# Performance work log

Hardware: AMD Instinct MI355X
Metric: run time of the kernel (lower is better)

Reference implementation:

```python
import jax, jax.numpy as jnp
import numpy as np


def setup_inputs() -> dict:
    key = jax.random.key(0)
    k1, k2, k3, k4 = jax.random.split(key, 4)
    B, Cin, Cout, K, Wd, H, Wsp = 16, 256, 256, 3, 256, 64, 64
    fan_in = Cin * K * K
    return {
        "x": jax.random.normal(k1, (B, Cin, H, Wsp), dtype=jnp.float32),
        "w": jax.random.normal(k2, (B, Wd), dtype=jnp.float32),
        "conv_weight": jax.random.normal(k3, (Cout, Cin, K, K), dtype=jnp.float32) * 0.05,
        "style_w": jax.random.normal(k4, (Cin, Wd), dtype=jnp.float32) * 0.05,
        "style_b": jnp.zeros((Cin,), dtype=jnp.float32),
        "scale": jnp.asarray(1.0 / np.sqrt(fan_in), dtype=jnp.float32),
    }


def reference(x, w, conv_weight, style_w, style_b, scale):
    # x: [B, Cin, H, W]; w: [B, Wd]; conv_weight: [Cout, Cin, K, K]
    B, Cin, H, Wsp = x.shape
    Cout, _, K, _ = conv_weight.shape
    # style modulation: s = Linear(w) -> [B, 1, Cin, 1, 1]
    s = (w @ style_w.T + style_b).reshape(B, 1, Cin, 1, 1)
    # modulate + demodulate per-sample weights: [B, Cout, Cin, K, K]
    wt = (conv_weight * scale)[None] * s
    demod = jax.lax.rsqrt(jnp.sum(wt * wt, axis=(2, 3, 4), keepdims=True) + 1e-8)
    wt = (wt * demod).reshape(B * Cout, Cin, K, K)
    # grouped conv emulation: input [1, B*Cin, H, W], groups=B
    xr = x.reshape(1, B * Cin, H, Wsp)
    pad = 1
    out = jax.lax.conv_general_dilated(
        xr, wt,
        window_strides=(1, 1),
        padding=[(pad, pad), (pad, pad)],
        dimension_numbers=("NCHW", "OIHW", "NCHW"),
        feature_group_count=B,
    )
    return out.reshape(B, Cout, out.shape[2], out.shape[3])
```

## Files before the change

### kernel.cpp

```cpp
#include <hip/hip_runtime.h>
#include <hip/hip_bf16.h>

#define BB   16
#define CIN  256
#define COUT 256
#define WD   256
#define HH   64
#define WWS  64
#define NSP  4096
#define KW   9

typedef __attribute__((ext_vector_type(8))) short short8;
typedef __attribute__((ext_vector_type(4))) float f32x4;
typedef unsigned short ushort_t;

#define S_BYTES (BB*CIN*4)
#define WT_OFF (S_BYTES)
#define WT_BYTES (BB*9*COUT*CIN*2)
#define X_OFF (WT_OFF + WT_BYTES)
#define X_BYTES (BB*NSP*CIN*2)
#define ZP_OFF (X_OFF + X_BYTES)
#define ZP_BYTES 4096
#define WS_NEEDED ((size_t)(ZP_OFF + ZP_BYTES))

#define WAITVM2 asm volatile("s_waitcnt vmcnt(2)" ::: "memory")
#define WAITVM8 asm volatile("s_waitcnt vmcnt(8)" ::: "memory")

__device__ inline ushort_t f2bf(float f) {
    __hip_bfloat16 h = __float2bfloat16(f);
    return __builtin_bit_cast(ushort_t, h);
}

__device__ inline void gload_lds16(const ushort_t* g, ushort_t* l) {
    __builtin_amdgcn_global_load_lds(
        (const __attribute__((address_space(1))) void*)g,
        (__attribute__((address_space(3))) void*)l, 16, 0, 0);
}

__global__ __launch_bounds__(256)
void zero_kernel(float* __restrict__ zp) {
    ((float4*)zp)[threadIdx.x] = make_float4(0.f, 0.f, 0.f, 0.f);
}

__global__ __launch_bounds__(256)
void style_kernel(const float* __restrict__ w,
                  const float* __restrict__ style_w,
                  const float* __restrict__ style_b,
                  float* __restrict__ s) {
    const int b  = blockIdx.x;
    const int ci = threadIdx.x;
    __shared__ float wsh[WD];
    wsh[ci] = w[b * WD + ci];
    __syncthreads();
    const float* row = style_w + ci * WD;
    float acc = style_b[ci];
    #pragma unroll 4
    for (int k = 0; k < WD; ++k) acc += wsh[k] * row[k];
    s[b * CIN + ci] = acc;
}

__global__ __launch_bounds__(256)
void wt_kernel(const float* __restrict__ cw, const float* __restrict__ s,
               const float* __restrict__ scale_p, ushort_t* __restrict__ wt) {
    const int co = blockIdx.x, b = blockIdx.y, ci = threadIdx.x;
    const float sv = s[b * CIN + ci] * scale_p[0];
    const float* cp = cw + ((size_t)co * CIN + ci) * KW;
    float v[9];
    float ss = 0.f;
    #pragma unroll
    for (int t = 0; t < 9; ++t) { v[t] = cp[t] * sv; ss += v[t] * v[t]; }
    #pragma unroll
    for (int off = 32; off > 0; off >>= 1) ss += __shfl_down(ss, off);
    __shared__ float red[4];
    if ((ci & 63) == 0) red[ci >> 6] = ss;
    __syncthreads();
    const float dm = rsqrtf(red[0] + red[1] + red[2] + red[3] + 1e-8f);
    #pragma unroll
    for (int t = 0; t < 9; ++t)
        wt[((size_t)(b * 9 + t) * COUT + co) * CIN + ci] = f2bf(v[t] * dm);
}

__global__ __launch_bounds__(256)
void xpose_kernel(const float* __restrict__ x, ushort_t* __restrict__ xo) {
    const int spt = blockIdx.x;
    const int cit = blockIdx.y;
    const int b   = blockIdx.z;
    const int t   = threadIdx.x;
    __shared__ ushort_t tile[64 * 68];
    const int sp0 = spt * 64, ci0 = cit * 64;
    {
        const int spq = t & 15, cil = t >> 4;
        #pragma unroll
        for (int i = 0; i < 4; ++i) {
            const int ci = cil + i * 16;
            const float4 v = *(const float4*)(x + ((size_t)(b * CIN + ci0 + ci)) * NSP + sp0 + spq * 4);
            tile[(spq * 4 + 0) * 68 + ci] = f2bf(v.x);
            tile[(spq * 4 + 1) * 68 + ci] = f2bf(v.y);
            tile[(spq * 4 + 2) * 68 + ci] = f2bf(v.z);
            tile[(spq * 4 + 3) * 68 + ci] = f2bf(v.w);
        }
    }
    __syncthreads();
    {
        const int g4 = t & 15, sp = t >> 4;
        #pragma unroll
        for (int i = 0; i < 4; ++i) {
            const int spp = sp + i * 16;
            uint2 v = *(const uint2*)&tile[spp * 68 + g4 * 4];
            *(uint2*)(xo + ((size_t)(b * NSP + sp0 + spp)) * CIN + ci0 + g4 * 4) = v;
        }
    }
}

__global__ __launch_bounds__(256, 2)
void conv_mfma_kernel(const ushort_t* __restrict__ wt,
                      const ushort_t* __restrict__ xo,
                      const ushort_t* __restrict__ zp,
                      float* __restrict__ out) {
    const int wg = blockIdx.x;
    const int b  = (wg & 7) + 8 * ((wg >> 3) & 1);
    const int cohalf = (wg >> 4) & 1;
    const int ntile  = wg >> 5;
    const int y0 = ntile * 4;

    const int tid  = threadIdx.x;
    const int lane = tid & 63;
    const int w    = tid >> 6;
    const int wm   = w >> 1;
    const int wn   = w & 1;
    const int l15  = lane & 15;
    const int lg   = lane >> 4;
    const int q    = lane >> 2;

    __shared__ __align__(16) ushort_t lds_a[3 * 128 * 32];
    __shared__ __align__(16) ushort_t lds_x[2 * 6 * 66 * 32];

    const int srcq8 = (((lane & 3) ^ ((q ^ (q >> 2)) & 3))) * 8;

    const long wtb = (long)b * 9 * COUT * CIN;
    const ushort_t* pa0 = wt + wtb + (long)(cohalf * 128 + w * 16 + q) * CIN + srcq8;
    const ushort_t* pa1 = pa0 + 64 * CIN;
    const int aluni0 = w * 512;
    const int aluni1 = 2048 + w * 512;

    const ushort_t* px[6];
    int xdst_off[6];
    #pragma unroll
    for (int j = 0; j < 6; ++j) {
        const int s  = w * 6 + j;
        const int r  = s >> 2;
        const int cq = s & 3;
        const int y  = y0 - 1 + r;
        const bool val = (y >= 0 && y < HH);
        const int cp = cq * 16 + q;
        px[j] = val ? (xo + ((long)b * NSP + (long)y * WWS + cp) * CIN + srcq8)
                    : (zp + lane * 8);
        xdst_off[j] = r * 2112 + cq * 512 + 32;
    }

    const int slotA8 = (lg ^ ((l15 ^ (l15 >> 2)) & 3)) * 8;
    int slotB8[3];
    #pragma unroll
    for (int kx = 0; kx < 3; ++kx) {
        int c2 = l15 + kx - 1;
        if (c2 < 0) c2 = 0;
        slotB8[kx] = (lg ^ ((c2 ^ (c2 >> 2)) & 3)) * 8;
    }
    const int abase = (wm * 64 + l15) * 32 + slotA8;

    f32x4 acc[4][8];
    #pragma unroll
    for (int mi = 0; mi < 4; ++mi)
        #pragma unroll
        for (int ni = 0; ni < 8; ++ni) acc[mi][ni] = (f32x4){0.f, 0.f, 0.f, 0.f};

    if (tid < 96) {
        const int cell = tid >> 2, qq = tid & 3;
        const int buf = cell / 12, cr = cell % 12;
        const int r = cr >> 1, col = (cr & 1) * 65;
        *(uint4*)&lds_x[buf * 12672 + r * 2112 + col * 32 + qq * 8] =
            make_uint4(0, 0, 0, 0);
    }

    #pragma unroll
    for (int j = 0; j < 6; ++j)
        gload_lds16(px[j], lds_x + xdst_off[j]);
    gload_lds16(pa0, lds_a + aluni0);
    gload_lds16(pa1, lds_a + aluni1);
    gload_lds16(pa0 + (long)COUT * CIN, lds_a + 4096 + aluni0);
    gload_lds16(pa1 + (long)COUT * CIN, lds_a + 4096 + aluni1);

    asm volatile("s_waitcnt lgkmcnt(0)" ::: "memory");

    for (int chunk = 0; chunk < 8; ++chunk) {
        const ushort_t* xb = lds_x + (chunk & 1) * 12672;

        #pragma unroll
        for (int tap = 0; tap < 9; ++tap) {
            if (tap == 1 || tap == 2) { WAITVM8; } else { WAITVM2; }
            __builtin_amdgcn_sched_barrier(0);
            __builtin_amdgcn_s_barrier();

            {
                const int tp2 = (tap + 2) % 9;
                const int ch2 = (tap >= 7) ? ((chunk + 1) & 7) : chunk;
                const long aoff = (long)tp2 * (COUT * CIN) + ch2 * 32;
                ushort_t* adst = lds_a + ((tap + 2) % 3) * 4096;
                gload_lds16(pa0 + aoff, adst + aluni0);
                gload_lds16(pa1 + aoff, adst + aluni1);
            }
            if (tap == 0) {
                const int cs = (chunk + 1) & 7;
                ushort_t* xdst = lds_x + ((chunk + 1) & 1) * 12672;
                #pragma unroll
                for (int j = 0; j < 6; ++j)
                    gload_lds16(px[j] + cs * 32, xdst + xdst_off[j]);
            }

            const int ky = tap / 3, kx = tap % 3;
            const ushort_t* ab = lds_a + (tap % 3) * 4096 + abase;
            short8 af[4];
            #pragma unroll
            for (int mi = 0; mi < 4; ++mi) af[mi] = *(const short8*)(ab + mi * 512);
            short8 bf[8];
            #pragma unroll
            for (int ni = 0; ni < 8; ++ni) {
                const int row = wn * 2 + (ni >> 2) + ky;
                const int col = (ni & 3) * 16 + l15 + kx;
                bf[ni] = *(const short8*)(xb + row * 2112 + col * 32 + slotB8[kx]);
            }

            __builtin_amdgcn_s_setprio(1);
            #pragma unroll
            for (int mi = 0; mi < 4; ++mi)
                #pragma unroll
                for (int ni = 0; ni < 8; ++ni)
                    acc[mi][ni] = __builtin_amdgcn_mfma_f32_16x16x32_bf16(
                        af[mi], bf[ni], acc[mi][ni], 0, 0, 0);
            __builtin_amdgcn_s_setprio(0);
        }
    }

    const int co_b = cohalf * 128 + wm * 64 + lg * 4;
    const int sp_b = ntile * 256 + wn * 128 + l15;
    #pragma unroll
    for (int mi = 0; mi < 4; ++mi)
        #pragma unroll
        for (int ni = 0; ni < 8; ++ni)
            #pragma unroll
            for (int rg = 0; rg < 4; ++rg) {
                const int co = co_b + mi * 16 + rg;
                const int sp = sp_b + ni * 16;
                out[((long)(b * COUT + co)) * NSP + sp] = acc[mi][ni][rg];
            }
}

__global__ __launch_bounds__(256)
void modconv_kernel(const float* __restrict__ x,
                    const float* __restrict__ cw,
                    const float* __restrict__ s,
                    const float* __restrict__ scale_p,
                    float* __restrict__ out) {
    const int tile = blockIdx.x;
    const int co   = blockIdx.y;
    const int b    = blockIdx.z;
    const int tid  = threadIdx.x;
    const float scale = scale_p[0];

    __shared__ float s_wt[CIN * KW];
    __shared__ float s_x[18 * 66];
    __shared__ float red[4];

    const float* cwb = cw + (size_t)co * CIN * KW;
    const float* sb  = s + b * CIN;
    float sumsq = 0.f;
    for (int i = tid; i < CIN * KW; i += 256) {
        float v = cwb[i] * scale * sb[i / KW];
        s_wt[i] = v;
        sumsq += v * v;
    }
    #pragma unroll
    for (int off = 32; off > 0; off >>= 1) sumsq += __shfl_down(sumsq, off);
    if ((tid & 63) == 0) red[tid >> 6] = sumsq;
    __syncthreads();
    const float demod = rsqrtf(red[0] + red[1] + red[2] + red[3] + 1e-8f);
    for (int i = tid; i < CIN * KW; i += 256) s_wt[i] *= demod;

    const int tx = tid & 63;
    const int tr = tid >> 6;
    const int y0 = tile * 16;
    float acc[4] = {0.f, 0.f, 0.f, 0.f};

    for (int ci = 0; ci < CIN; ++ci) {
        __syncthreads();
        const float* xb = x + ((size_t)(b * CIN + ci)) * (HH * WWS);
        for (int idx = tid; idx < 18 * 66; idx += 256) {
            const int r = idx / 66, c = idx % 66;
            const int yg = y0 - 1 + r, xg = c - 1;
            float v = 0.f;
            if (yg >= 0 && yg < HH && xg >= 0 && xg < WWS) v = xb[yg * WWS + xg];
            s_x[idx] = v;
        }
        __syncthreads();
        const float* wr = s_wt + ci * KW;
        const float w0 = wr[0], w1 = wr[1], w2 = wr[2];
        const float w3 = wr[3], w4 = wr[4], w5 = wr[5];
        const float w6 = wr[6], w7 = wr[7], w8 = wr[8];
        const int rbase = tr * 4;
        float xv[6][3];
        #pragma unroll
        for (int j = 0; j < 6; ++j)
            #pragma unroll
            for (int k = 0; k < 3; ++k) xv[j][k] = s_x[(rbase + j) * 66 + tx + k];
        #pragma unroll
        for (int i = 0; i < 4; ++i)
            acc[i] += w0 * xv[i][0] + w1 * xv[i][1] + w2 * xv[i][2]
                    + w3 * xv[i+1][0] + w4 * xv[i+1][1] + w5 * xv[i+1][2]
                    + w6 * xv[i+2][0] + w7 * xv[i+2][1] + w8 * xv[i+2][2];
    }
    float* ob = out + (((size_t)(b * COUT + co)) * HH + y0) * WWS + tx;
    #pragma unroll
    for (int i = 0; i < 4; ++i) ob[(tr * 4 + i) * WWS] = acc[i];
}

extern "C" void kernel_launch(void* const* d_in, const int* in_sizes, int n_in,
                              void* d_out, int out_size, void* d_ws, size_t ws_size,
                              hipStream_t stream) {
    const float* x       = (const float*)d_in[0];
    const float* w       = (const float*)d_in[1];
    const float* cw      = (const float*)d_in[2];
    const float* style_w = (const float*)d_in[3];
    const float* style_b = (const float*)d_in[4];
    const float* scale_p = (const float*)d_in[5];
    float*       out     = (float*)d_out;

    float*    s    = (float*)d_ws;
    ushort_t* wswt = (ushort_t*)((char*)d_ws + WT_OFF);
    ushort_t* wsx  = (ushort_t*)((char*)d_ws + X_OFF);
    float*    zp   = (float*)((char*)d_ws + ZP_OFF);

    style_kernel<<<dim3(BB), 256, 0, stream>>>(w, style_w, style_b, s);

    if (ws_size >= WS_NEEDED) {
        zero_kernel<<<dim3(1), 256, 0, stream>>>(zp);
        wt_kernel<<<dim3(COUT, BB), 256, 0, stream>>>(cw, s, scale_p, wswt);
        xpose_kernel<<<dim3(64, 4, BB), 256, 0, stream>>>(x, wsx);
        conv_mfma_kernel<<<dim3(512), 256, 0, stream>>>(wswt, wsx,
                                                        (const ushort_t*)zp, out);
    } else {
        modconv_kernel<<<dim3(4, COUT, BB), 256, 0, stream>>>(x, cw, s, scale_p, out);
    }
}
```

Measured before the change: 108.7 us.

## Enlarge conv tile to all 256 output channels per workgroup with vectorized stores

Each workgroup now computes all 256 output channels for its spatial tile instead of half, so the input halo tile is loaded once per spatial tile rather than twice, and the grid halves to 256 workgroups. Each wave holds a 128x128 accumulator block, which raises register pressure and drops occupancy to one workgroup per SIMD set. The MFMA operands are swapped so each lane holds four consecutive spatial outputs, which turns the epilogue into 16-byte vector stores. Wait counts and LDS buffer sizes are adjusted for the doubled weight loads.

Result: slower. 131.4 us (+20.8%).

```diff
diff --git a/kernel.cpp b/kernel.cpp
--- a/kernel.cpp
+++ b/kernel.cpp
@@ -23,8 +23,8 @@
 #define ZP_BYTES 4096
 #define WS_NEEDED ((size_t)(ZP_OFF + ZP_BYTES))
 
-#define WAITVM2 asm volatile("s_waitcnt vmcnt(2)" ::: "memory")
-#define WAITVM8 asm volatile("s_waitcnt vmcnt(8)" ::: "memory")
+#define WAITVM4  asm volatile("s_waitcnt vmcnt(4)" ::: "memory")
+#define WAITVM10 asm volatile("s_waitcnt vmcnt(10)" ::: "memory")
 
 __device__ inline ushort_t f2bf(float f) {
     __hip_bfloat16 h = __float2bfloat16(f);
@@ -112,15 +112,14 @@
     }
 }
 
-__global__ __launch_bounds__(256, 2)
+__global__ __launch_bounds__(256, 1)
 void conv_mfma_kernel(const ushort_t* __restrict__ wt,
                       const ushort_t* __restrict__ xo,
                       const ushort_t* __restrict__ zp,
                       float* __restrict__ out) {
     const int wg = blockIdx.x;
-    const int b  = (wg & 7) + 8 * ((wg >> 3) & 1);
-    const int cohalf = (wg >> 4) & 1;
-    const int ntile  = wg >> 5;
+    const int b  = (wg & 7) | ((wg >> 7) << 3);
+    const int ntile = (wg >> 3) & 15;
     const int y0 = ntile * 4;
 
     const int tid  = threadIdx.x;
@@ -132,16 +131,19 @@
     const int lg   = lane >> 4;
     const int q    = lane >> 2;
 
-    __shared__ __align__(16) ushort_t lds_a[3 * 128 * 32];
+    __shared__ __align__(16) ushort_t lds_a[3 * 256 * 32];
     __shared__ __align__(16) ushort_t lds_x[2 * 6 * 66 * 32];
 
     const int srcq8 = (((lane & 3) ^ ((q ^ (q >> 2)) & 3))) * 8;
 
     const long wtb = (long)b * 9 * COUT * CIN;
-    const ushort_t* pa0 = wt + wtb + (long)(cohalf * 128 + w * 16 + q) * CIN + srcq8;
-    const ushort_t* pa1 = pa0 + 64 * CIN;
-    const int aluni0 = w * 512;
-    const int aluni1 = 2048 + w * 512;
+    const ushort_t* pa[4];
+    int aluni[4];
+    #pragma unroll
+    for (int i = 0; i < 4; ++i) {
+        pa[i] = wt + wtb + (long)(i * 64 + w * 16 + q) * CIN + srcq8;
+        aluni[i] = i * 2048 + w * 512;
+    }
 
     const ushort_t* px[6];
     int xdst_off[6];
@@ -166,11 +168,11 @@
         if (c2 < 0) c2 = 0;
         slotB8[kx] = (lg ^ ((c2 ^ (c2 >> 2)) & 3)) * 8;
     }
-    const int abase = (wm * 64 + l15) * 32 + slotA8;
-
-    f32x4 acc[4][8];
-    #pragma unroll
-    for (int mi = 0; mi < 4; ++mi)
+    const int abase = (wm * 128 + l15) * 32 + slotA8;
+
+    f32x4 acc[8][8];
+    #pragma unroll
+    for (int mi = 0; mi < 8; ++mi)
         #pragma unroll
         for (int ni = 0; ni < 8; ++ni) acc[mi][ni] = (f32x4){0.f, 0.f, 0.f, 0.f};
 
@@ -181,23 +183,25 @@
         *(uint4*)&lds_x[buf * 12672 + r * 2112 + col * 32 + qq * 8] =
             make_uint4(0, 0, 0, 0);
     }
+    asm volatile("s_waitcnt lgkmcnt(0)" ::: "memory");
+    __builtin_amdgcn_sched_barrier(0);
 
     #pragma unroll
     for (int j = 0; j < 6; ++j)
         gload_lds16(px[j], lds_x + xdst_off[j]);
-    gload_lds16(pa0, lds_a + aluni0);
-    gload_lds16(pa1, lds_a + aluni1);
-    gload_lds16(pa0 + (long)COUT * CIN, lds_a + 4096 + aluni0);
-    gload_lds16(pa1 + (long)COUT * CIN, lds_a + 4096 + aluni1);
-
-    asm volatile("s_waitcnt lgkmcnt(0)" ::: "memory");
+    #pragma unroll
+    for (int i = 0; i < 4; ++i)
+        gload_lds16(pa[i], lds_a + aluni[i]);
+    #pragma unroll
+    for (int i = 0; i < 4; ++i)
+        gload_lds16(pa[i] + (long)COUT * CIN, lds_a + 8192 + aluni[i]);
 
     for (int chunk = 0; chunk < 8; ++chunk) {
         const ushort_t* xb = lds_x + (chunk & 1) * 12672;
 
         #pragma unroll
         for (int tap = 0; tap < 9; ++tap) {
-            if (tap == 1 || tap == 2) { WAITVM8; } else { WAITVM2; }
+            if (tap == 1 || tap == 2) { WAITVM10; } else { WAITVM4; }
             __builtin_amdgcn_sched_barrier(0);
             __builtin_amdgcn_s_barrier();
 
@@ -205,9 +209,10 @@
                 const int tp2 = (tap + 2) % 9;
                 const int ch2 = (tap >= 7) ? ((chunk + 1) & 7) : chunk;
                 const long aoff = (long)tp2 * (COUT * CIN) + ch2 * 32;
-                ushort_t* adst = lds_a + ((tap + 2) % 3) * 4096;
-                gload_lds16(pa0 + aoff, adst + aluni0);
-                gload_lds16(pa1 + aoff, adst + aluni1);
+                ushort_t* adst = lds_a + ((tap + 2) % 3) * 8192;
+                #pragma unroll
+                for (int i = 0; i < 4; ++i)
+                    gload_lds16(pa[i] + aoff, adst + aluni[i]);
             }
             if (tap == 0) {
                 const int cs = (chunk + 1) & 7;
@@ -218,10 +223,10 @@
             }
 
             const int ky = tap / 3, kx = tap % 3;
-            const ushort_t* ab = lds_a + (tap % 3) * 4096 + abase;
-            short8 af[4];
+            const ushort_t* ab = lds_a + (tap % 3) * 8192 + abase;
+            short8 af[8];
             #pragma unroll
-            for (int mi = 0; mi < 4; ++mi) af[mi] = *(const short8*)(ab + mi * 512);
+            for (int mi = 0; mi < 8; ++mi) af[mi] = *(const short8*)(ab + mi * 512);
             short8 bf[8];
             #pragma unroll
             for (int ni = 0; ni < 8; ++ni) {
@@ -232,27 +237,24 @@
 
             __builtin_amdgcn_s_setprio(1);
             #pragma unroll
-            for (int mi = 0; mi < 4; ++mi)
+            for (int mi = 0; mi < 8; ++mi)
                 #pragma unroll
                 for (int ni = 0; ni < 8; ++ni)
                     acc[mi][ni] = __builtin_amdgcn_mfma_f32_16x16x32_bf16(
-                        af[mi], bf[ni], acc[mi][ni], 0, 0, 0);
+                        bf[ni], af[mi], acc[mi][ni], 0, 0, 0);
             __builtin_amdgcn_s_setprio(0);
         }
     }
 
-    const int co_b = cohalf * 128 + wm * 64 + lg * 4;
-    const int sp_b = ntile * 256 + wn * 128 + l15;
-    #pragma unroll
-    for (int mi = 0; mi < 4; ++mi)
+    #pragma unroll
+    for (int mi = 0; mi < 8; ++mi) {
+        const int co = wm * 128 + mi * 16 + l15;
+        float* ob = out + ((long)(b * COUT + co)) * NSP
+                  + ntile * 256 + wn * 128 + lg * 4;
         #pragma unroll
         for (int ni = 0; ni < 8; ++ni)
-            #pragma unroll
-            for (int rg = 0; rg < 4; ++rg) {
-                const int co = co_b + mi * 16 + rg;
-                const int sp = sp_b + ni * 16;
-                out[((long)(b * COUT + co)) * NSP + sp] = acc[mi][ni][rg];
-            }
+            *(f32x4*)(ob + ni * 16) = acc[mi][ni];
+    }
 }
 
 __global__ __launch_bounds__(256)
@@ -345,7 +347,7 @@
         zero_kernel<<<dim3(1), 256, 0, stream>>>(zp);
         wt_kernel<<<dim3(COUT, BB), 256, 0, stream>>>(cw, s, scale_p, wswt);
         xpose_kernel<<<dim3(64, 4, BB), 256, 0, stream>>>(x, wsx);
-        conv_mfma_kernel<<<dim3(512), 256, 0, stream>>>(wswt, wsx,
+        conv_mfma_kernel<<<dim3(256), 256, 0, stream>>>(wswt, wsx,
                                                         (const ushort_t*)zp, out);
     } else {
         modconv_kernel<<<dim3(4, COUT, BB), 256, 0, stream>>>(x, cw, s, scale_p, out);
```

## Split conv workgroup across 8 waves with smaller per-wave tiles and vector stores

Applied to the files above, without the earlier changes.

Doubles the conv kernel's workgroup to 512 threads (8 waves), halving each wave's accumulator tile to 4x4 MFMA blocks and the number of async global-to-LDS loads per thread. The MFMA operands are swapped so each lane holds four consecutive spatial outputs, which lets the epilogue write 16-byte vector stores instead of scalar ones. The vmcnt wait counts are lowered to match the fewer in-flight loads. This aims for more latency hiding and less register pressure, at the cost of more barrier participants and less register-level reuse per wave.

After: 110.3 us. No clear change (+1.5%).

```diff
diff --git a/kernel.cpp b/kernel.cpp
--- a/kernel.cpp
+++ b/kernel.cpp
@@ -23,8 +23,8 @@
 #define ZP_BYTES 4096
 #define WS_NEEDED ((size_t)(ZP_OFF + ZP_BYTES))
 
-#define WAITVM2 asm volatile("s_waitcnt vmcnt(2)" ::: "memory")
-#define WAITVM8 asm volatile("s_waitcnt vmcnt(8)" ::: "memory")
+#define WAITVM1 asm volatile("s_waitcnt vmcnt(1)" ::: "memory")
+#define WAITVM4 asm volatile("s_waitcnt vmcnt(4)" ::: "memory")
 
 __device__ inline ushort_t f2bf(float f) {
     __hip_bfloat16 h = __float2bfloat16(f);
@@ -112,22 +112,23 @@
     }
 }
 
-__global__ __launch_bounds__(256, 2)
+__global__ __launch_bounds__(512, 4)
 void conv_mfma_kernel(const ushort_t* __restrict__ wt,
                       const ushort_t* __restrict__ xo,
                       const ushort_t* __restrict__ zp,
                       float* __restrict__ out) {
     const int wg = blockIdx.x;
-    const int b  = (wg & 7) + 8 * ((wg >> 3) & 1);
-    const int cohalf = (wg >> 4) & 1;
-    const int ntile  = wg >> 5;
+    const int b  = (wg & 7) | (((wg >> 3) & 1) << 3);
+    const int r2 = wg >> 4;
+    const int cohalf = r2 & 1;
+    const int ntile  = r2 >> 1;
     const int y0 = ntile * 4;
 
     const int tid  = threadIdx.x;
     const int lane = tid & 63;
     const int w    = tid >> 6;
-    const int wm   = w >> 1;
-    const int wn   = w & 1;
+    const int wm   = w >> 2;
+    const int wn   = w & 3;
     const int l15  = lane & 15;
     const int lg   = lane >> 4;
     const int q    = lane >> 2;
@@ -135,27 +136,25 @@
     __shared__ __align__(16) ushort_t lds_a[3 * 128 * 32];
     __shared__ __align__(16) ushort_t lds_x[2 * 6 * 66 * 32];
 
-    const int srcq8 = (((lane & 3) ^ ((q ^ (q >> 2)) & 3))) * 8;
-
+    const int srcqA8 = ((lane & 3) ^ ((q ^ (q >> 2)) & 3)) * 8;
     const long wtb = (long)b * 9 * COUT * CIN;
-    const ushort_t* pa0 = wt + wtb + (long)(cohalf * 128 + w * 16 + q) * CIN + srcq8;
-    const ushort_t* pa1 = pa0 + 64 * CIN;
-    const int aluni0 = w * 512;
-    const int aluni1 = 2048 + w * 512;
-
-    const ushort_t* px[6];
-    int xdst_off[6];
-    #pragma unroll
-    for (int j = 0; j < 6; ++j) {
-        const int s  = w * 6 + j;
-        const int r  = s >> 2;
-        const int cq = s & 3;
-        const int y  = y0 - 1 + r;
+    const ushort_t* pa = wt + wtb + (long)(cohalf * 128 + w * 16 + q) * CIN + srcqA8;
+    const int aluni = w * 512;
+
+    const ushort_t* px[3];
+    int xdst_off[3];
+    #pragma unroll
+    for (int j = 0; j < 3; ++j) {
+        const int idx = j * 8 + w;
+        const int r   = idx >> 2;
+        const int cg  = idx & 3;
+        const int col = cg * 16 + (lane >> 2);
+        const int sq8 = ((lane & 3) ^ ((col ^ (col >> 2)) & 3)) * 8;
+        const int y   = y0 - 1 + r;
         const bool val = (y >= 0 && y < HH);
-        const int cp = cq * 16 + q;
-        px[j] = val ? (xo + ((long)b * NSP + (long)y * WWS + cp) * CIN + srcq8)
+        px[j] = val ? (xo + ((long)b * NSP + (long)y * WWS + col) * CIN + sq8)
                     : (zp + lane * 8);
-        xdst_off[j] = r * 2112 + cq * 512 + 32;
+        xdst_off[j] = r * 2112 + (cg * 16 + 1) * 32;
     }
 
     const int slotA8 = (lg ^ ((l15 ^ (l15 >> 2)) & 3)) * 8;
@@ -168,11 +167,11 @@
     }
     const int abase = (wm * 64 + l15) * 32 + slotA8;
 
-    f32x4 acc[4][8];
+    f32x4 acc[4][4];
     #pragma unroll
     for (int mi = 0; mi < 4; ++mi)
         #pragma unroll
-        for (int ni = 0; ni < 8; ++ni) acc[mi][ni] = (f32x4){0.f, 0.f, 0.f, 0.f};
+        for (int ni = 0; ni < 4; ++ni) acc[mi][ni] = (f32x4){0.f, 0.f, 0.f, 0.f};
 
     if (tid < 96) {
         const int cell = tid >> 2, qq = tid & 3;
@@ -181,23 +180,21 @@
         *(uint4*)&lds_x[buf * 12672 + r * 2112 + col * 32 + qq * 8] =
             make_uint4(0, 0, 0, 0);
     }
-
-    #pragma unroll
-    for (int j = 0; j < 6; ++j)
+    asm volatile("s_waitcnt lgkmcnt(0)" ::: "memory");
+    __builtin_amdgcn_sched_barrier(0);
+
+    #pragma unroll
+    for (int j = 0; j < 3; ++j)
         gload_lds16(px[j], lds_x + xdst_off[j]);
-    gload_lds16(pa0, lds_a + aluni0);
-    gload_lds16(pa1, lds_a + aluni1);
-    gload_lds16(pa0 + (long)COUT * CIN, lds_a + 4096 + aluni0);
-    gload_lds16(pa1 + (long)COUT * CIN, lds_a + 4096 + aluni1);
-
-    asm volatile("s_waitcnt lgkmcnt(0)" ::: "memory");
+    gload_lds16(pa, lds_a + aluni);
+    gload_lds16(pa + (long)COUT * CIN, lds_a + 4096 + aluni);
 
     for (int chunk = 0; chunk < 8; ++chunk) {
         const ushort_t* xb = lds_x + (chunk & 1) * 12672;
 
         #pragma unroll
         for (int tap = 0; tap < 9; ++tap) {
-            if (tap == 1 || tap == 2) { WAITVM8; } else { WAITVM2; }
+            if (tap == 1 || tap == 2) { WAITVM4; } else { WAITVM1; }
             __builtin_amdgcn_sched_barrier(0);
             __builtin_amdgcn_s_barrier();
 
@@ -205,15 +202,13 @@
                 const int tp2 = (tap + 2) % 9;
                 const int ch2 = (tap >= 7) ? ((chunk + 1) & 7) : chunk;
                 const long aoff = (long)tp2 * (COUT * CIN) + ch2 * 32;
-                ushort_t* adst = lds_a + ((tap + 2) % 3) * 4096;
-                gload_lds16(pa0 + aoff, adst + aluni0);
-                gload_lds16(pa1 + aoff, adst + aluni1);
+                gload_lds16(pa + aoff, lds_a + ((tap + 2) % 3) * 4096 + aluni);
             }
             if (tap == 0) {
                 const int cs = (chunk + 1) & 7;
                 ushort_t* xdst = lds_x + ((chunk + 1) & 1) * 12672;
                 #pragma unroll
-                for (int j = 0; j < 6; ++j)
+                for (int j = 0; j < 3; ++j)
                     gload_lds16(px[j] + cs * 32, xdst + xdst_off[j]);
             }
 
@@ -222,11 +217,11 @@
             short8 af[4];
             #pragma unroll
             for (int mi = 0; mi < 4; ++mi) af[mi] = *(const short8*)(ab + mi * 512);
-            short8 bf[8];
+            short8 bf[4];
             #pragma unroll
-            for (int ni = 0; ni < 8; ++ni) {
-                const int row = wn * 2 + (ni >> 2) + ky;
-                const int col = (ni & 3) * 16 + l15 + kx;
+            for (int ni = 0; ni < 4; ++ni) {
+                const int row = wn + ky;
+                const int col = ni * 16 + l15 + kx;
                 bf[ni] = *(const short8*)(xb + row * 2112 + col * 32 + slotB8[kx]);
             }
 
@@ -234,25 +229,22 @@
             #pragma unroll
             for (int mi = 0; mi < 4; ++mi)
                 #pragma unroll
-                for (int ni = 0; ni < 8; ++ni)
+                for (int ni = 0; ni < 4; ++ni)
                     acc[mi][ni] = __builtin_amdgcn_mfma_f32_16x16x32_bf16(
-                        af[mi], bf[ni], acc[mi][ni], 0, 0, 0);
+                        bf[ni], af[mi], acc[mi][ni], 0, 0, 0);
             __builtin_amdgcn_s_setprio(0);
         }
     }
 
-    const int co_b = cohalf * 128 + wm * 64 + lg * 4;
-    const int sp_b = ntile * 256 + wn * 128 + l15;
-    #pragma unroll
-    for (int mi = 0; mi < 4; ++mi)
-        #pragma unroll
-        for (int ni = 0; ni < 8; ++ni)
-            #pragma unroll
-            for (int rg = 0; rg < 4; ++rg) {
-                const int co = co_b + mi * 16 + rg;
-                const int sp = sp_b + ni * 16;
-                out[((long)(b * COUT + co)) * NSP + sp] = acc[mi][ni][rg];
-            }
+    #pragma unroll
+    for (int mi = 0; mi < 4; ++mi) {
+        const int co = cohalf * 128 + wm * 64 + mi * 16 + l15;
+        float* ob = out + ((long)(b * COUT + co)) * NSP
+                  + ntile * 256 + wn * 64 + lg * 4;
+        #pragma unroll
+        for (int ni = 0; ni < 4; ++ni)
+            *(f32x4*)(ob + ni * 16) = acc[mi][ni];
+    }
 }
 
 __global__ __launch_bounds__(256)
@@ -345,7 +337,7 @@
         zero_kernel<<<dim3(1), 256, 0, stream>>>(zp);
         wt_kernel<<<dim3(COUT, BB), 256, 0, stream>>>(cw, s, scale_p, wswt);
         xpose_kernel<<<dim3(64, 4, BB), 256, 0, stream>>>(x, wsx);
-        conv_mfma_kernel<<<dim3(512), 256, 0, stream>>>(wswt, wsx,
+        conv_mfma_kernel<<<dim3(512), 512, 0, stream>>>(wswt, wsx,
                                                         (const ushort_t*)zp, out);
     } else {
         modconv_kernel<<<dim3(4, COUT, BB), 256, 0, stream>>>(x, cw, s, scale_p, out);
```
